# Kernel optimization log

Measured on AMD Instinct MI355X. Metric: run time of the kernel, lower is better.

## Reference

```python
import jax, jax.numpy as jnp
import numpy as np

# 5x5 binomial Gaussian kernel, normalized by 256
_K = jnp.array([[1., 4., 6., 4., 1.],
                [4., 16., 24., 16., 4.],
                [6., 24., 36., 24., 6.],
                [4., 16., 24., 16., 4.],
                [1., 4., 6., 4., 1.]], dtype=jnp.float32) / 256.0


def _gauss_conv(img, kernel):
    # depthwise 5x5 conv with reflect padding 2 (same spatial size)
    C = img.shape[1]
    p = jnp.pad(img, ((0, 0), (0, 0), (2, 2), (2, 2)), mode='reflect')
    return jax.lax.conv_general_dilated(
        p, kernel, window_strides=(1, 1), padding='VALID',
        dimension_numbers=('NCHW', 'OIHW', 'NCHW'),
        feature_group_count=C)


def _lap_pyramid(img, kernel, max_levels=5):
    pyr = []
    cur = img
    for _ in range(max_levels):  # fixed small loop over pyramid levels
        H, W = cur.shape[2], cur.shape[3]
        cur = cur[:, :, :H - H % 2, :W - W % 2]  # crop to even size
        down = _gauss_conv(cur, kernel)[:, :, ::2, ::2]
        up = jnp.zeros(cur.shape, cur.dtype).at[:, :, ::2, ::2].set(down * 4.0)
        up = _gauss_conv(up, kernel)
        pyr.append(cur - up)
        cur = down
    return pyr


def setup_inputs() -> dict:
    key = jax.random.key(0)
    k1, k2 = jax.random.split(key)
    predict = jax.random.uniform(k1, (16, 3, 512, 512), dtype=jnp.float32)
    target = jax.random.uniform(k2, (16, 3, 512, 512), dtype=jnp.float32)
    return {"predict": predict, "target": target}


def reference(predict, target):
    C = predict.shape[1]
    kernel = jnp.tile(_K.astype(predict.dtype)[None, None], (C, 1, 1, 1))  # [C,1,5,5]
    pyr_p = _lap_pyramid(predict, kernel, 5)
    pyr_t = _lap_pyramid(target, kernel, 5)
    weights = (1.0, 2.0, 4.0, 8.0, 16.0)
    loss = jnp.asarray(0.0, predict.dtype)
    for w, a, b in zip(weights, pyr_p, pyr_t):
        loss = loss + w * jnp.mean(jnp.abs(a - b))  # F.l1_loss (mean reduction)
    return loss
```

## Files before the change

kernel.cpp:

```cpp
#include <hip/hip_runtime.h>


__device__ __forceinline__ int reflect_i(int m, int S) {
    if (m < 0) m = -m;
    if (m >= S) m = 2 * S - 2 - m;
    return m;
}

__device__ __forceinline__ void wg_barrier() {
    asm volatile("s_waitcnt lgkmcnt(0)" ::: "memory");
    __builtin_amdgcn_s_barrier();
}

#define LGKM0 asm volatile("s_waitcnt lgkmcnt(0)" ::: "memory")

template <int N>
__device__ __forceinline__ void wait_vm() {
    if constexpr (N == 0)      asm volatile("s_waitcnt vmcnt(0)" ::: "memory");
    else if constexpr (N == 1) asm volatile("s_waitcnt vmcnt(1)" ::: "memory");
    else if constexpr (N == 2) asm volatile("s_waitcnt vmcnt(2)" ::: "memory");
    else if constexpr (N == 4) asm volatile("s_waitcnt vmcnt(4)" ::: "memory");
    else if constexpr (N == 8) asm volatile("s_waitcnt vmcnt(8)" ::: "memory");
}

__device__ __forceinline__ void gld16(const void* g, void* l) {
    __builtin_amdgcn_global_load_lds(
        (const __attribute__((address_space(1))) void*)g,
        (__attribute__((address_space(3))) void*)l, 16, 0, 0);
}

template <int S, int ISL0, int DH, int WPB>
__global__ __launch_bounds__(WPB * 64, 2)
void pyr_kernel(const float* __restrict__ a, const float* __restrict__ b,
                float* __restrict__ dwn, float* __restrict__ acc, float scale) {
    constexpr int D = S / 2;
    constexpr int CPL = S / 128;
    constexpr int ROWB = (CPL == 4) ? 2048 : 1024;
    constexpr int SLOT = ROWB * (ISL0 ? 2 : 1);
    constexpr int OPS = (CPL == 4) ? (ISL0 ? 4 : 2) : 1;
    constexpr int NRS = D / DH;

    __shared__ float4 ringmem[WPB * 4 * SLOT / 16];
    const int wv = threadIdx.x >> 6;
    const int lane = threadIdx.x & 63;
    char* ring = (char*)ringmem + wv * (4 * SLOT);

    const int wid = blockIdx.x * WPB + wv;
    const int rs = wid % NRS;
    const int n = wid / NRS;
    const int R0 = rs * DH;
    const size_t gbase = (size_t)n * S * S;

    auto stage_row = [&](int s) {
        int gr = reflect_i(2 * R0 - 4 + s, S);
        const char* ga = (const char*)(a + gbase + (size_t)gr * S);
        char* la = ring + (s & 3) * SLOT;
        if constexpr (CPL == 4) {
            gld16(ga + 16 * lane, la);
            gld16(ga + 16 * lane + 1024, la + 1024);
        } else if constexpr (CPL == 2) {
            gld16(ga + 16 * lane, la);
        } else {
            gld16(ga + 16 * (lane & 31), la);
        }
        if constexpr (ISL0) {
            const char* gb = (const char*)(b + gbase + (size_t)gr * S);
            gld16(gb + 16 * lane, la + ROWB);
            gld16(gb + 16 * lane + 1024, la + ROWB + 1024);
        }
    };

    auto proc_row = [&](int s, float* c, float* h) {
        const char* pa = ring + (s & 3) * SLOT;
        if constexpr (CPL == 4) {
            float4 x0 = *(const float4*)(pa + 16 * lane);
            float4 x1 = *(const float4*)(pa + 1024 + 16 * lane);
            if constexpr (ISL0) {
                const char* pb = pa + ROWB;
                float4 y0 = *(const float4*)(pb + 16 * lane);
                float4 y1 = *(const float4*)(pb + 1024 + 16 * lane);
                x0.x -= y0.x; x0.y -= y0.y; x0.z -= y0.z; x0.w -= y0.w;
                x1.x -= y1.x; x1.y -= y1.y; x1.z -= y1.z; x1.w -= y1.w;
            }
            c[0]=x0.x; c[1]=x0.y; c[2]=x0.z; c[3]=x0.w;
            c[4]=x1.x; c[5]=x1.y; c[6]=x1.z; c[7]=x1.w;
            float lu2  = __shfl_up(x0.z, 1, 64);
            float lu3  = __shfl_up(x0.w, 1, 64);
            float rd0  = __shfl_down(x0.x, 1, 64);
            float bcA  = __shfl(x1.x, 0, 64);
            float lu2b = __shfl_up(x1.z, 1, 64);
            float lu3b = __shfl_up(x1.w, 1, 64);
            float rd0b = __shfl_down(x1.x, 1, 64);
            float bcZ  = __shfl(x0.z, 63, 64);
            float bcW  = __shfl(x0.w, 63, 64);
            float w0 = (lane == 0) ? x0.z : lu2;
            float w1 = (lane == 0) ? x0.y : lu3;
            float w6 = (lane == 63) ? bcA : rd0;
            float v0 = (lane == 0) ? bcZ : lu2b;
            float v1 = (lane == 0) ? bcW : lu3b;
            float v6 = (lane == 63) ? x1.z : rd0b;
            h[0] = w0 + 4.f*w1 + 6.f*x0.x + 4.f*x0.y + x0.z;
            h[1] = x0.x + 4.f*x0.y + 6.f*x0.z + 4.f*x0.w + w6;
            h[2] = v0 + 4.f*v1 + 6.f*x1.x + 4.f*x1.y + x1.z;
            h[3] = x1.x + 4.f*x1.y + 6.f*x1.z + 4.f*x1.w + v6;
        } else if constexpr (CPL == 2) {
            float4 x0 = *(const float4*)(pa + 16 * lane);
            c[0]=x0.x; c[1]=x0.y; c[2]=x0.z; c[3]=x0.w;
            float lu2 = __shfl_up(x0.z, 1, 64);
            float lu3 = __shfl_up(x0.w, 1, 64);
            float rd0 = __shfl_down(x0.x, 1, 64);
            float w0 = (lane == 0) ? x0.z : lu2;
            float w1 = (lane == 0) ? x0.y : lu3;
            float w6 = (lane == 63) ? x0.z : rd0;
            h[0] = w0 + 4.f*w1 + 6.f*x0.x + 4.f*x0.y + x0.z;
            h[1] = x0.x + 4.f*x0.y + 6.f*x0.z + 4.f*x0.w + w6;
        } else {
            float2 x0 = *(const float2*)(pa + 8 * lane);
            c[0]=x0.x; c[1]=x0.y;
            float lu0 = __shfl_up(x0.x, 1, 64);
            float lu1 = __shfl_up(x0.y, 1, 64);
            float rd0 = __shfl_down(x0.x, 1, 64);
            float w0 = (lane == 0) ? rd0 : lu0;
            float w1 = (lane == 0) ? x0.y : lu1;
            float w4 = (lane == 63) ? x0.x : rd0;
            h[0] = w0 + 4.f*w1 + 6.f*x0.x + 4.f*x0.y + w4;
        }
    };

    float hA[CPL], hB[CPL], hC[CPL], hD[CPL], hE[CPL];
    float cEv1[2*CPL], cEv2[2*CPL], cOd1[2*CPL], dump[2*CPL];
    float ex0[CPL] = {}, ex1[CPL] = {}, ox0[CPL] = {}, ox1[CPL] = {};
    float sum = 0.f;
    float* dbase = dwn + (size_t)n * D * D;

    stage_row(0); stage_row(1); stage_row(2); stage_row(3);
    wait_vm<OPS>();
    proc_row(0, dump, hA);
    proc_row(1, dump, hB);
    proc_row(2, dump, hC);
    LGKM0;
    stage_row(4); stage_row(5); stage_row(6);

    #pragma unroll
    for (int j = 0; j <= DH + 1; ++j) {
        const int m = R0 - 1 + j;
        if (j <= DH) wait_vm<2 * OPS>(); else wait_vm<0>();

        float c3[2*CPL], c4[2*CPL];
        proc_row(2 * j + 3, c3, hD);
        proc_row(2 * j + 4, c4, hE);

        float d[CPL], dl[CPL], dr[CPL], ex2[CPL], ox2[CPL];
        #pragma unroll
        for (int q = 0; q < CPL; q++)
            d[q] = (hA[q] + 4.f*hB[q] + 6.f*hC[q] + 4.f*hD[q] + hE[q]) * (1.f / 256.f);

        if constexpr (CPL == 4) {
            float su1 = __shfl_up(d[1], 1, 64);
            float su3 = __shfl_up(d[3], 1, 64);
            float sd0 = __shfl_down(d[0], 1, 64);
            float sd2 = __shfl_down(d[2], 1, 64);
            float bc1 = __shfl(d[1], 63, 64);
            float bc2 = __shfl(d[2], 0, 64);
            dl[0] = (lane == 0) ? d[1] : su1;
            dl[1] = d[0];
            dl[2] = (lane == 0) ? bc1 : su3;
            dl[3] = d[2];
            dr[0] = d[1];
            dr[1] = (lane == 63) ? bc2 : sd0;
            dr[2] = d[3];
            dr[3] = (lane == 63) ? d[3] : sd2;
        } else if constexpr (CPL == 2) {
            float su1 = __shfl_up(d[1], 1, 64);
            float sd0 = __shfl_down(d[0], 1, 64);
            dl[0] = (lane == 0) ? d[1] : su1;
            dl[1] = d[0];
            dr[0] = d[1];
            dr[1] = (lane == 63) ? d[1] : sd0;
        } else {
            float su = __shfl_up(d[0], 1, 64);
            float sd = __shfl_down(d[0], 1, 64);
            dl[0] = (lane == 0) ? sd : su;
            dr[0] = (lane == 63) ? d[0] : sd;
        }
        #pragma unroll
        for (int q = 0; q < CPL; q++) {
            ex2[q] = 0.125f * (dl[q] + 6.f * d[q] + dr[q]);
            ox2[q] = 0.5f * (d[q] + dr[q]);
        }

        if (j >= 1 && j <= DH) {
            if constexpr (CPL == 4) {
                *(float2*)(dbase + (size_t)m * D + 2 * lane) = make_float2(d[0], d[1]);
                *(float2*)(dbase + (size_t)m * D + D / 2 + 2 * lane) = make_float2(d[2], d[3]);
            } else if constexpr (CPL == 2) {
                *(float2*)(dbase + (size_t)m * D + 2 * lane) = make_float2(d[0], d[1]);
            } else {
                dbase[(size_t)m * D + lane] = d[0];
            }
        }

        if (j >= 2) {
            const int me = m - 1;
            #pragma unroll
            for (int q = 0; q < CPL; q++) {
                float eA = (me == 0) ? ex2[q] : ex0[q];
                float oA = (me == 0) ? ox2[q] : ox0[q];
                float eC = (me == D - 1) ? ex1[q] : ex2[q];
                float oC = (me == D - 1) ? ox1[q] : ox2[q];
                float uee = 0.125f * (eA + 6.f * ex1[q] + eC);
                float ueo = 0.125f * (oA + 6.f * ox1[q] + oC);
                float uoe = 0.5f * (ex1[q] + eC);
                float uoo = 0.5f * (ox1[q] + oC);
                sum += fabsf(cEv2[2*q]   - uee) + fabsf(cEv2[2*q+1] - ueo)
                     + fabsf(cOd1[2*q]   - uoe) + fabsf(cOd1[2*q+1] - uoo);
            }
        }

        #pragma unroll
        for (int q = 0; q < CPL; q++) {
            ex0[q] = ex1[q]; ex1[q] = ex2[q];
            ox0[q] = ox1[q]; ox1[q] = ox2[q];
            hA[q] = hC[q]; hB[q] = hD[q]; hC[q] = hE[q];
        }
        #pragma unroll
        for (int q = 0; q < 2 * CPL; q++) {
            cEv2[q] = cEv1[q];
            cEv1[q] = c4[q];
            cOd1[q] = c3[q];
        }

        if (j <= DH - 1) {
            LGKM0;
            stage_row(2 * j + 7);
            stage_row(2 * j + 8);
        }
    }

    #pragma unroll
    for (int o = 32; o > 0; o >>= 1) sum += __shfl_down(sum, o, 64);
    if (lane == 0) atomicAdd(&acc[wid & 63], sum * scale);
}

__device__ float level_in_lds(const float* cur, float* h, float* dn,
                              int S, int tid, int nt) {
    const int D = S >> 1;
    for (int i = tid; i < S * D; i += nt) {
        int r = i / D, xh = i % D;
        int c0 = reflect_i(2 * xh - 2, S), c1 = reflect_i(2 * xh - 1, S);
        int c3 = 2 * xh + 1, c4 = reflect_i(2 * xh + 2, S);
        const float* row = cur + r * S;
        h[i] = row[c0] + 4.f * row[c1] + 6.f * row[2 * xh] + 4.f * row[c3] + row[c4];
    }
    wg_barrier();
    for (int i = tid; i < D * D; i += nt) {
        int yh = i / D, xh = i % D;
        int r0 = reflect_i(2 * yh - 2, S), r1 = reflect_i(2 * yh - 1, S);
        int r3 = 2 * yh + 1, r4 = reflect_i(2 * yh + 2, S);
        dn[i] = (h[r0 * D + xh] + 4.f * h[r1 * D + xh] + 6.f * h[2 * yh * D + xh]
               + 4.f * h[r3 * D + xh] + h[r4 * D + xh]) * (1.f / 256.f);
    }
    wg_barrier();
    float sum = 0.f;
    for (int i = tid; i < D * D; i += nt) {
        int yh2 = i / D, q = i % D;
        int rm = (yh2 == 0) ? 1 : yh2 - 1;
        int rp = (yh2 == D - 1) ? D - 1 : yh2 + 1;
        int cm = (q == 0) ? 1 : q - 1;
        int cp = (q == D - 1) ? D - 1 : q + 1;
        float A00 = dn[rm * D + cm], A01 = dn[rm * D + q], A02 = dn[rm * D + cp];
        float A10 = dn[yh2 * D + cm], A11 = dn[yh2 * D + q], A12 = dn[yh2 * D + cp];
        float A20 = dn[rp * D + cm], A21 = dn[rp * D + q], A22 = dn[rp * D + cp];
        float ex0 = (A00 + 6.f * A01 + A02) * 0.125f;
        float ex1 = (A10 + 6.f * A11 + A12) * 0.125f;
        float ex2 = (A20 + 6.f * A21 + A22) * 0.125f;
        float ox0 = (A01 + A02) * 0.5f;
        float ox1 = (A11 + A12) * 0.5f;
        float ox2 = (A21 + A22) * 0.5f;
        float uee = (ex0 + 6.f * ex1 + ex2) * 0.125f;
        float ueo = (ox0 + 6.f * ox1 + ox2) * 0.125f;
        float uoe = (ex1 + ex2) * 0.5f;
        float uoo = (ox1 + ox2) * 0.5f;
        const float* c0 = cur + (2 * yh2) * S + 2 * q;
        sum += fabsf(c0[0] - uee) + fabsf(c0[1] - ueo)
             + fabsf(c0[S] - uoe) + fabsf(c0[S + 1] - uoo);
    }
    wg_barrier();
    return sum;
}

__global__ __launch_bounds__(512, 1)
void tail_kernel(const float* __restrict__ d1, float* __restrict__ acc,
                 float s2, float s3, float s4) {
    __shared__ float cur[128 * 128];
    __shared__ float hbuf[128 * 64];
    __shared__ float dn2[64 * 64];
    int n = blockIdx.x, tid = threadIdx.x;
    const int nt = 512;
    const float4* src = (const float4*)(d1 + (size_t)n * 128 * 128);
    for (int i = tid; i < 128 * 32; i += nt) ((float4*)cur)[i] = src[i];
    wg_barrier();
    float sum = level_in_lds(cur, hbuf, dn2, 128, tid, nt) * s2;
    float* dn3 = cur;
    sum += level_in_lds(dn2, hbuf, dn3, 64, tid, nt) * s3;
    float* dn4 = cur + 32 * 32;
    sum += level_in_lds(dn3, hbuf, dn4, 32, tid, nt) * s4;
    #pragma unroll
    for (int o = 32; o > 0; o >>= 1) sum += __shfl_down(sum, o, 64);
    __shared__ float s[8];
    int lane = tid & 63, w = tid >> 6;
    if (lane == 0) s[w] = sum;
    wg_barrier();
    if (tid == 0) {
        float v = 0.f;
        #pragma unroll
        for (int i = 0; i < 8; i++) v += s[i];
        atomicAdd(&acc[n & 63], v);
    }
}

__global__ void finish_kernel(const float* __restrict__ acc, float* __restrict__ out) {
    float v = acc[threadIdx.x];
    #pragma unroll
    for (int o = 32; o > 0; o >>= 1) v += __shfl_down(v, o, 64);
    if (threadIdx.x == 0) out[0] = v;
}

extern "C" void kernel_launch(void* const* d_in, const int* in_sizes, int n_in,
                              void* d_out, int out_size, void* d_ws, size_t ws_size,
                              hipStream_t stream) {
    const float* p = (const float*)d_in[0];
    const float* t = (const float*)d_in[1];
    float* out = (float*)d_out;
    float* acc = (float*)d_ws;
    float* dn0 = acc + 64;
    float* dn1 = dn0 + (size_t)48 * 256 * 256;

    hipMemsetAsync(acc, 0, 64 * sizeof(float), stream);

    const int N = 48;

    pyr_kernel<512, 1, 16, 2><<<384, 128, 0, stream>>>(
        p, t, dn0, acc, 1.f / (float)(N * 512 * 512));
    pyr_kernel<256, 0, 8, 4><<<192, 256, 0, stream>>>(
        dn0, nullptr, dn1, acc, 2.f / (float)(N * 256 * 256));
    tail_kernel<<<N, 512, 0, stream>>>(dn1, acc,
                                       4.f / (float)(N * 128 * 128),
                                       8.f / (float)(N * 64 * 64),
                                       16.f / (float)(N * 32 * 32));
    finish_kernel<<<1, 64, 0, stream>>>(acc, out);
}
```

Baseline: 56.83 us.

## Process two independent row strips per wavefront to raise memory-level parallelism

Each wavefront now handles two row strips (NB=2) at once. It interleaves the global-to-LDS loads and per-row compute of both strips, so twice as many loads are in flight and waits overlap. For level 0 the strip height is halved to keep the grid size, and level 1 uses half as many blocks. The change doubles LDS and register use per wave and drops the min-blocks launch bound hint, which may reduce occupancy.

```diff
diff --git a/kernel.cpp b/kernel.cpp
--- a/kernel.cpp
+++ b/kernel.cpp
@@ -16,11 +16,11 @@
 
 template <int N>
 __device__ __forceinline__ void wait_vm() {
-    if constexpr (N == 0)      asm volatile("s_waitcnt vmcnt(0)" ::: "memory");
-    else if constexpr (N == 1) asm volatile("s_waitcnt vmcnt(1)" ::: "memory");
-    else if constexpr (N == 2) asm volatile("s_waitcnt vmcnt(2)" ::: "memory");
-    else if constexpr (N == 4) asm volatile("s_waitcnt vmcnt(4)" ::: "memory");
-    else if constexpr (N == 8) asm volatile("s_waitcnt vmcnt(8)" ::: "memory");
+    if constexpr (N == 0)       asm volatile("s_waitcnt vmcnt(0)" ::: "memory");
+    else if constexpr (N == 2)  asm volatile("s_waitcnt vmcnt(2)" ::: "memory");
+    else if constexpr (N == 4)  asm volatile("s_waitcnt vmcnt(4)" ::: "memory");
+    else if constexpr (N == 8)  asm volatile("s_waitcnt vmcnt(8)" ::: "memory");
+    else if constexpr (N == 16) asm volatile("s_waitcnt vmcnt(16)" ::: "memory");
 }
 
 __device__ __forceinline__ void gld16(const void* g, void* l) {
@@ -30,9 +30,10 @@
 }
 
 template <int S, int ISL0, int DH, int WPB>
-__global__ __launch_bounds__(WPB * 64, 2)
-void pyr_kernel(const float* __restrict__ a, const float* __restrict__ b,
-                float* __restrict__ dwn, float* __restrict__ acc, float scale) {
+__global__ __launch_bounds__(WPB * 64)
+void pyr2_kernel(const float* __restrict__ a, const float* __restrict__ b,
+                 float* __restrict__ dwn, float* __restrict__ acc, float scale) {
+    constexpr int NB = 2;
     constexpr int D = S / 2;
     constexpr int CPL = S / 128;
     constexpr int ROWB = (CPL == 4) ? 2048 : 1024;
@@ -40,38 +41,43 @@
     constexpr int OPS = (CPL == 4) ? (ISL0 ? 4 : 2) : 1;
     constexpr int NRS = D / DH;
 
-    __shared__ float4 ringmem[WPB * 4 * SLOT / 16];
+    __shared__ float4 ringmem[WPB * NB * 4 * SLOT / 16];
     const int wv = threadIdx.x >> 6;
     const int lane = threadIdx.x & 63;
-    char* ring = (char*)ringmem + wv * (4 * SLOT);
+    char* ringw = (char*)ringmem + wv * (NB * 4 * SLOT);
 
     const int wid = blockIdx.x * WPB + wv;
-    const int rs = wid % NRS;
-    const int n = wid / NRS;
-    const int R0 = rs * DH;
-    const size_t gbase = (size_t)n * S * S;
-
-    auto stage_row = [&](int s) {
-        int gr = reflect_i(2 * R0 - 4 + s, S);
-        const char* ga = (const char*)(a + gbase + (size_t)gr * S);
-        char* la = ring + (s & 3) * SLOT;
+    int R0[NB];
+    size_t gbase[NB], dboff[NB];
+    #pragma unroll
+    for (int k = 0; k < NB; k++) {
+        int g = wid * NB + k;
+        int rs = g % NRS;
+        int n = g / NRS;
+        R0[k] = rs * DH;
+        gbase[k] = (size_t)n * S * S;
+        dboff[k] = (size_t)n * D * D;
+    }
+
+    auto stage_row = [&](int k, int s) {
+        int gr = reflect_i(2 * R0[k] - 4 + s, S);
+        const char* ga = (const char*)(a + gbase[k] + (size_t)gr * S);
+        char* la = ringw + k * (4 * SLOT) + (s & 3) * SLOT;
         if constexpr (CPL == 4) {
             gld16(ga + 16 * lane, la);
             gld16(ga + 16 * lane + 1024, la + 1024);
-        } else if constexpr (CPL == 2) {
+        } else {
             gld16(ga + 16 * lane, la);
-        } else {
-            gld16(ga + 16 * (lane & 31), la);
         }
         if constexpr (ISL0) {
-            const char* gb = (const char*)(b + gbase + (size_t)gr * S);
+            const char* gb = (const char*)(b + gbase[k] + (size_t)gr * S);
             gld16(gb + 16 * lane, la + ROWB);
             gld16(gb + 16 * lane + 1024, la + ROWB + 1024);
         }
     };
 
-    auto proc_row = [&](int s, float* c, float* h) {
-        const char* pa = ring + (s & 3) * SLOT;
+    auto proc_row = [&](int k, int s, float* c, float* h) {
+        const char* pa = ringw + k * (4 * SLOT) + (s & 3) * SLOT;
         if constexpr (CPL == 4) {
             float4 x0 = *(const float4*)(pa + 16 * lane);
             float4 x1 = *(const float4*)(pa + 1024 + 16 * lane);
@@ -103,7 +109,7 @@
             h[1] = x0.x + 4.f*x0.y + 6.f*x0.z + 4.f*x0.w + w6;
             h[2] = v0 + 4.f*v1 + 6.f*x1.x + 4.f*x1.y + x1.z;
             h[3] = x1.x + 4.f*x1.y + 6.f*x1.z + 4.f*x1.w + v6;
-        } else if constexpr (CPL == 2) {
+        } else {
             float4 x0 = *(const float4*)(pa + 16 * lane);
             c[0]=x0.x; c[1]=x0.y; c[2]=x0.z; c[3]=x0.w;
             float lu2 = __shfl_up(x0.z, 1, 64);
@@ -114,126 +120,121 @@
             float w6 = (lane == 63) ? x0.z : rd0;
             h[0] = w0 + 4.f*w1 + 6.f*x0.x + 4.f*x0.y + x0.z;
             h[1] = x0.x + 4.f*x0.y + 6.f*x0.z + 4.f*x0.w + w6;
-        } else {
-            float2 x0 = *(const float2*)(pa + 8 * lane);
-            c[0]=x0.x; c[1]=x0.y;
-            float lu0 = __shfl_up(x0.x, 1, 64);
-            float lu1 = __shfl_up(x0.y, 1, 64);
-            float rd0 = __shfl_down(x0.x, 1, 64);
-            float w0 = (lane == 0) ? rd0 : lu0;
-            float w1 = (lane == 0) ? x0.y : lu1;
-            float w4 = (lane == 63) ? x0.x : rd0;
-            h[0] = w0 + 4.f*w1 + 6.f*x0.x + 4.f*x0.y + w4;
         }
     };
 
-    float hA[CPL], hB[CPL], hC[CPL], hD[CPL], hE[CPL];
-    float cEv1[2*CPL], cEv2[2*CPL], cOd1[2*CPL], dump[2*CPL];
-    float ex0[CPL] = {}, ex1[CPL] = {}, ox0[CPL] = {}, ox1[CPL] = {};
+    float hA[NB][CPL], hB[NB][CPL], hC[NB][CPL], hD[NB][CPL], hE[NB][CPL];
+    float cEv1[NB][2*CPL], cEv2[NB][2*CPL], cOd1[NB][2*CPL], dump[2*CPL];
+    float ex0[NB][CPL] = {}, ex1[NB][CPL] = {}, ox0[NB][CPL] = {}, ox1[NB][CPL] = {};
     float sum = 0.f;
-    float* dbase = dwn + (size_t)n * D * D;
-
-    stage_row(0); stage_row(1); stage_row(2); stage_row(3);
-    wait_vm<OPS>();
-    proc_row(0, dump, hA);
-    proc_row(1, dump, hB);
-    proc_row(2, dump, hC);
+
+    #pragma unroll
+    for (int s = 0; s < 4; s++) { stage_row(0, s); stage_row(1, s); }
+    wait_vm<2 * OPS>();
+    #pragma unroll
+    for (int k = 0; k < NB; k++) {
+        proc_row(k, 0, dump, hA[k]);
+        proc_row(k, 1, dump, hB[k]);
+        proc_row(k, 2, dump, hC[k]);
+    }
     LGKM0;
-    stage_row(4); stage_row(5); stage_row(6);
+    #pragma unroll
+    for (int s = 4; s < 7; s++) { stage_row(0, s); stage_row(1, s); }
 
     #pragma unroll
     for (int j = 0; j <= DH + 1; ++j) {
-        const int m = R0 - 1 + j;
-        if (j <= DH) wait_vm<2 * OPS>(); else wait_vm<0>();
-
-        float c3[2*CPL], c4[2*CPL];
-        proc_row(2 * j + 3, c3, hD);
-        proc_row(2 * j + 4, c4, hE);
-
-        float d[CPL], dl[CPL], dr[CPL], ex2[CPL], ox2[CPL];
+        if (j <= DH) wait_vm<4 * OPS>(); else wait_vm<0>();
+
+        float c3[NB][2*CPL], c4[NB][2*CPL];
         #pragma unroll
-        for (int q = 0; q < CPL; q++)
-            d[q] = (hA[q] + 4.f*hB[q] + 6.f*hC[q] + 4.f*hD[q] + hE[q]) * (1.f / 256.f);
-
-        if constexpr (CPL == 4) {
-            float su1 = __shfl_up(d[1], 1, 64);
-            float su3 = __shfl_up(d[3], 1, 64);
-            float sd0 = __shfl_down(d[0], 1, 64);
-            float sd2 = __shfl_down(d[2], 1, 64);
-            float bc1 = __shfl(d[1], 63, 64);
-            float bc2 = __shfl(d[2], 0, 64);
-            dl[0] = (lane == 0) ? d[1] : su1;
-            dl[1] = d[0];
-            dl[2] = (lane == 0) ? bc1 : su3;
-            dl[3] = d[2];
-            dr[0] = d[1];
-            dr[1] = (lane == 63) ? bc2 : sd0;
-            dr[2] = d[3];
-            dr[3] = (lane == 63) ? d[3] : sd2;
-        } else if constexpr (CPL == 2) {
-            float su1 = __shfl_up(d[1], 1, 64);
-            float sd0 = __shfl_down(d[0], 1, 64);
-            dl[0] = (lane == 0) ? d[1] : su1;
-            dl[1] = d[0];
-            dr[0] = d[1];
-            dr[1] = (lane == 63) ? d[1] : sd0;
-        } else {
-            float su = __shfl_up(d[0], 1, 64);
-            float sd = __shfl_down(d[0], 1, 64);
-            dl[0] = (lane == 0) ? sd : su;
-            dr[0] = (lane == 63) ? d[0] : sd;
-        }
+        for (int k = 0; k < NB; k++) {
+            proc_row(k, 2 * j + 3, c3[k], hD[k]);
+            proc_row(k, 2 * j + 4, c4[k], hE[k]);
+        }
+
         #pragma unroll
-        for (int q = 0; q < CPL; q++) {
-            ex2[q] = 0.125f * (dl[q] + 6.f * d[q] + dr[q]);
-            ox2[q] = 0.5f * (d[q] + dr[q]);
-        }
-
-        if (j >= 1 && j <= DH) {
+        for (int k = 0; k < NB; k++) {
+            const int m = R0[k] - 1 + j;
+            float d[CPL], dl[CPL], dr[CPL], ex2[CPL], ox2[CPL];
+            #pragma unroll
+            for (int q = 0; q < CPL; q++)
+                d[q] = (hA[k][q] + 4.f*hB[k][q] + 6.f*hC[k][q]
+                      + 4.f*hD[k][q] + hE[k][q]) * (1.f / 256.f);
+
             if constexpr (CPL == 4) {
-                *(float2*)(dbase + (size_t)m * D + 2 * lane) = make_float2(d[0], d[1]);
-                *(float2*)(dbase + (size_t)m * D + D / 2 + 2 * lane) = make_float2(d[2], d[3]);
-            } else if constexpr (CPL == 2) {
-                *(float2*)(dbase + (size_t)m * D + 2 * lane) = make_float2(d[0], d[1]);
+                float su1 = __shfl_up(d[1], 1, 64);
+                float su3 = __shfl_up(d[3], 1, 64);
+                float sd0 = __shfl_down(d[0], 1, 64);
+                float sd2 = __shfl_down(d[2], 1, 64);
+                float bc1 = __shfl(d[1], 63, 64);
+                float bc2 = __shfl(d[2], 0, 64);
+                dl[0] = (lane == 0) ? d[1] : su1;
+                dl[1] = d[0];
+                dl[2] = (lane == 0) ? bc1 : su3;
+                dl[3] = d[2];
+                dr[0] = d[1];
+                dr[1] = (lane == 63) ? bc2 : sd0;
+                dr[2] = d[3];
+                dr[3] = (lane == 63) ? d[3] : sd2;
             } else {
-                dbase[(size_t)m * D + lane] = d[0];
-            }
-        }
-
-        if (j >= 2) {
-            const int me = m - 1;
+                float su1 = __shfl_up(d[1], 1, 64);
+                float sd0 = __shfl_down(d[0], 1, 64);
+                dl[0] = (lane == 0) ? d[1] : su1;
+                dl[1] = d[0];
+                dr[0] = d[1];
+                dr[1] = (lane == 63) ? d[1] : sd0;
+            }
             #pragma unroll
             for (int q = 0; q < CPL; q++) {
-                float eA = (me == 0) ? ex2[q] : ex0[q];
-                float oA = (me == 0) ? ox2[q] : ox0[q];
-                float eC = (me == D - 1) ? ex1[q] : ex2[q];
-                float oC = (me == D - 1) ? ox1[q] : ox2[q];
-                float uee = 0.125f * (eA + 6.f * ex1[q] + eC);
-                float ueo = 0.125f * (oA + 6.f * ox1[q] + oC);
-                float uoe = 0.5f * (ex1[q] + eC);
-                float uoo = 0.5f * (ox1[q] + oC);
-                sum += fabsf(cEv2[2*q]   - uee) + fabsf(cEv2[2*q+1] - ueo)
-                     + fabsf(cOd1[2*q]   - uoe) + fabsf(cOd1[2*q+1] - uoo);
-            }
-        }
-
-        #pragma unroll
-        for (int q = 0; q < CPL; q++) {
-            ex0[q] = ex1[q]; ex1[q] = ex2[q];
-            ox0[q] = ox1[q]; ox1[q] = ox2[q];
-            hA[q] = hC[q]; hB[q] = hD[q]; hC[q] = hE[q];
-        }
-        #pragma unroll
-        for (int q = 0; q < 2 * CPL; q++) {
-            cEv2[q] = cEv1[q];
-            cEv1[q] = c4[q];
-            cOd1[q] = c3[q];
+                ex2[q] = 0.125f * (dl[q] + 6.f * d[q] + dr[q]);
+                ox2[q] = 0.5f * (d[q] + dr[q]);
+            }
+
+            if (j >= 1 && j <= DH) {
+                float* db = dwn + dboff[k];
+                if constexpr (CPL == 4) {
+                    *(float2*)(db + (size_t)m * D + 2 * lane) = make_float2(d[0], d[1]);
+                    *(float2*)(db + (size_t)m * D + D / 2 + 2 * lane) = make_float2(d[2], d[3]);
+                } else {
+                    *(float2*)(db + (size_t)m * D + 2 * lane) = make_float2(d[0], d[1]);
+                }
+            }
+
+            if (j >= 2) {
+                const int me = m - 1;
+                #pragma unroll
+                for (int q = 0; q < CPL; q++) {
+                    float eA = (me == 0) ? ex2[q] : ex0[k][q];
+                    float oA = (me == 0) ? ox2[q] : ox0[k][q];
+                    float eC = (me == D - 1) ? ex1[k][q] : ex2[q];
+                    float oC = (me == D - 1) ? ox1[k][q] : ox2[q];
+                    float uee = 0.125f * (eA + 6.f * ex1[k][q] + eC);
+                    float ueo = 0.125f * (oA + 6.f * ox1[k][q] + oC);
+                    float uoe = 0.5f * (ex1[k][q] + eC);
+                    float uoo = 0.5f * (ox1[k][q] + oC);
+                    sum += fabsf(cEv2[k][2*q]   - uee) + fabsf(cEv2[k][2*q+1] - ueo)
+                         + fabsf(cOd1[k][2*q]   - uoe) + fabsf(cOd1[k][2*q+1] - uoo);
+                }
+            }
+
+            #pragma unroll
+            for (int q = 0; q < CPL; q++) {
+                ex0[k][q] = ex1[k][q]; ex1[k][q] = ex2[q];
+                ox0[k][q] = ox1[k][q]; ox1[k][q] = ox2[q];
+                hA[k][q] = hC[k][q]; hB[k][q] = hD[k][q]; hC[k][q] = hE[k][q];
+            }
+            #pragma unroll
+            for (int q = 0; q < 2 * CPL; q++) {
+                cEv2[k][q] = cEv1[k][q];
+                cEv1[k][q] = c4[k][q];
+                cOd1[k][q] = c3[k][q];
+            }
         }
 
         if (j <= DH - 1) {
             LGKM0;
-            stage_row(2 * j + 7);
-            stage_row(2 * j + 8);
+            stage_row(0, 2 * j + 7); stage_row(1, 2 * j + 7);
+            stage_row(0, 2 * j + 8); stage_row(1, 2 * j + 8);
         }
     }
 
@@ -340,9 +341,9 @@
 
     const int N = 48;
 
-    pyr_kernel<512, 1, 16, 2><<<384, 128, 0, stream>>>(
+    pyr2_kernel<512, 1, 8, 2><<<384, 128, 0, stream>>>(
         p, t, dn0, acc, 1.f / (float)(N * 512 * 512));
-    pyr_kernel<256, 0, 8, 4><<<192, 256, 0, stream>>>(
+    pyr2_kernel<256, 0, 8, 4><<<96, 256, 0, stream>>>(
         dn0, nullptr, dn1, acc, 2.f / (float)(N * 256 * 256));
     tail_kernel<<<N, 512, 0, stream>>>(dn1, acc,
                                        4.f / (float)(N * 128 * 128),
```

New measurement: 60.45 us. 6.4% more time.
